# Performance work log

Measured on AMD Instinct MI355X. Metric: run time of the kernel, lower is better.

Reference implementation:

```python
import jax, jax.numpy as jnp
import numpy as np

HEADS = 4
DIM_HEAD = 32
SCALE = 10.0
EPS = 1e-12


def setup_inputs() -> dict:
    key = jax.random.key(0)
    k1, k2, k3 = jax.random.split(key, 3)
    B, D, H, W, C = 2, 8, 16, 32, 128
    dim = HEADS * DIM_HEAD  # 128
    x = jax.random.normal(k1, (B, D, H, W, C), dtype=jnp.float32)
    # 1x1x1 convs are matmuls over the channel dim
    w_qkv = jax.random.normal(k2, (C, 3 * dim), dtype=jnp.float32) * (1.0 / np.sqrt(C))
    w_out = jax.random.normal(k3, (dim, C), dtype=jnp.float32) * (1.0 / np.sqrt(dim))
    b_out = jnp.zeros((C,), dtype=jnp.float32)
    return {"x": x, "w_qkv": w_qkv, "w_out": w_out, "b_out": b_out}


def reference(x, w_qkv, w_out, b_out):
    B, D, H, W, C = x.shape
    N = D * H * W
    dim = HEADS * DIM_HEAD
    xf = x.reshape(B, N, C)
    qkv = xf @ w_qkv                                   # [B, N, 3*dim]
    q, k, v = jnp.split(qkv, 3, axis=-1)
    def to_heads(t):
        return t.reshape(B, N, HEADS, DIM_HEAD)        # [B, N, h, d]
    q, k, v = to_heads(q), to_heads(k), to_heads(v)
    # L2-normalize q and k along head dim (cosine attention)
    q = q / jnp.clip(jnp.linalg.norm(q, axis=-1, keepdims=True), EPS)
    k = k / jnp.clip(jnp.linalg.norm(k, axis=-1, keepdims=True), EPS)
    sim = jnp.einsum('bihd,bjhd->bhij', q, k) * SCALE  # [B, h, N, N]
    attn = jax.nn.softmax(sim, axis=-1)
    out = jnp.einsum('bhij,bjhd->bihd', attn, v)       # [B, N, h, d]
    out = out.reshape(B, N, dim)
    out = out @ w_out + b_out                          # [B, N, C]
    return out.reshape(B, D, H, W, C)
```

## Files before the change

### kernel.cpp

```cpp
#include <hip/hip_runtime.h>
#include <math.h>

#define HEADS   4
#define DH      32
#define NB      4096
#define BATCH   2
#define C_IN    128
#define QKV_COLS 384
#define TOTROWS 8192
#define ATT_EPS 1e-12f
#define C1      14.42695040888963f
#define QROWS   8
#define OROWS   8

typedef __attribute__((ext_vector_type(16))) float f32x16;
typedef _Float16 f16x8 __attribute__((ext_vector_type(8)));
typedef __fp16 fp16x2 __attribute__((ext_vector_type(2)));
typedef unsigned short u16;

__device__ __forceinline__ u16 f16b(float a) {
  union { _Float16 h; u16 u; } t; t.h = (_Float16)a; return t.u;
}
__device__ __forceinline__ unsigned pkf16rtn(float a, float b) {
  return (unsigned)f16b(a) | ((unsigned)f16b(b) << 16);
}
union Uh2 { fp16x2 h; unsigned u; };
__device__ __forceinline__ unsigned pkf16(float a, float b) {
  Uh2 t; t.h = __builtin_amdgcn_cvt_pkrtz(a, b); return t.u;
}
union U8h { unsigned u[4]; f16x8 h8; };
__device__ __forceinline__ f16x8 mk8h(unsigned a, unsigned b, unsigned c, unsigned d) {
  U8h t; t.u[0] = a; t.u[1] = b; t.u[2] = c; t.u[3] = d; return t.h8;
}
__device__ __forceinline__ void pl32swap(unsigned& a, unsigned& b) {
  asm("v_permlane32_swap_b32 %0, %1" : "+v"(a), "+v"(b));
}
#define GL16(gp, lp)                                                        \
  __builtin_amdgcn_global_load_lds(                                         \
      (const __attribute__((address_space(1))) void*)(gp),                  \
      (__attribute__((address_space(3))) void*)(lp), 16, 0, 0)

__global__ __launch_bounds__(384) void qkv_kernel(
    const float* __restrict__ x, const float* __restrict__ w,
    float* __restrict__ Qs, u16* __restrict__ K16, u16* __restrict__ VT16) {
  const int tid = threadIdx.x;
  const int r0  = blockIdx.x * QROWS;

  float4 a4[QROWS];
#pragma unroll
  for (int r = 0; r < QROWS; ++r) a4[r] = make_float4(0.f, 0.f, 0.f, 0.f);

  for (int c4 = 0; c4 < 32; ++c4) {
    const float wv0 = w[(c4 * 4 + 0) * QKV_COLS + tid];
    const float wv1 = w[(c4 * 4 + 1) * QKV_COLS + tid];
    const float wv2 = w[(c4 * 4 + 2) * QKV_COLS + tid];
    const float wv3 = w[(c4 * 4 + 3) * QKV_COLS + tid];
#pragma unroll
    for (int r = 0; r < QROWS; ++r) {
      const float* xr = x + (size_t)(r0 + r) * C_IN + c4 * 4;
      a4[r].x = fmaf(xr[0], wv0, a4[r].x);
      a4[r].y = fmaf(xr[1], wv1, a4[r].y);
      a4[r].z = fmaf(xr[2], wv2, a4[r].z);
      a4[r].w = fmaf(xr[3], wv3, a4[r].w);
    }
  }

  float acc[QROWS];
#pragma unroll
  for (int r = 0; r < QROWS; ++r)
    acc[r] = (a4[r].x + a4[r].y) + (a4[r].z + a4[r].w);

  const int part = tid >> 7;
  if (part < 2) {
#pragma unroll
    for (int r = 0; r < QROWS; ++r) {
      float s = acc[r] * acc[r];
      s += __shfl_xor(s, 1, 32);
      s += __shfl_xor(s, 2, 32);
      s += __shfl_xor(s, 4, 32);
      s += __shfl_xor(s, 8, 32);
      s += __shfl_xor(s, 16, 32);
      acc[r] *= 1.0f / fmaxf(sqrtf(s), ATT_EPS);
    }
  }

  const int h = (tid >> 5) & 3, d = tid & 31;
  const int b = r0 >> 12, n0 = r0 & (NB - 1);
  const int bh = b * HEADS + h;
  if (part == 0) {
    float* dst = Qs + ((size_t)bh * NB + n0) * DH + d;
#pragma unroll
    for (int r = 0; r < QROWS; ++r) dst[(size_t)r * DH] = acc[r] * C1;
  } else if (part == 1) {
    const size_t kb = ((size_t)bh * NB + n0) * DH + d;
#pragma unroll
    for (int r = 0; r < QROWS; ++r) K16[kb + (size_t)r * DH] = f16b(acc[r]);
  } else {
    const size_t vb = ((size_t)bh * DH + d) * NB + n0;
#pragma unroll
    for (int r = 0; r < QROWS; r += 4) {
      uint2 hv;
      hv.x = pkf16rtn(acc[r + 0], acc[r + 1]);
      hv.y = pkf16rtn(acc[r + 2], acc[r + 3]);
      *(uint2*)(VT16 + vb + r) = hv;
    }
  }
}

__global__ __launch_bounds__(512, 4) void attn_kernel(
    const float* __restrict__ Qs, const u16* __restrict__ K16,
    const u16* __restrict__ VT16, float* __restrict__ AO) {
  __shared__ __align__(16) char sbuf[2][4][2][2048];

  const int tid  = threadIdx.x;
  const int lane = tid & 63;
  const int w    = tid >> 6;
  const int su   = w & 3;
  const int u    = w >> 2;
  const int q    = lane & 31;
  const int hi   = lane >> 5;
  const int bh   = blockIdx.x & 7;
  const int qp   = blockIdx.x >> 3;

  const int nrow = qp * 64 + u * 32 + q;
  const float* qrow = Qs + ((size_t)bh * NB + nrow) * DH;
  f16x8 fq16[2];
#pragma unroll
  for (int sl = 0; sl < 2; ++sl) {
    const int d0 = sl * 16 + hi * 8;
    const float4 a = *(const float4*)(qrow + d0);
    const float4 b = *(const float4*)(qrow + d0 + 4);
    fq16[sl] = mk8h(pkf16rtn(a.x, a.y), pkf16rtn(a.z, a.w),
                    pkf16rtn(b.x, b.y), pkf16rtn(b.z, b.w));
  }

  const u16* gp[2]; int gst[2], ldso[2];
#pragma unroll
  for (int it = 0; it < 2; ++it) {
    const int i    = tid + it * 512;
    const int pidx = i >> 7;
    const int sp   = pidx >> 1;
    const int pl   = pidx & 1;
    const int s    = i & 127;
    const int rtt  = s >> 2;
    const int ps   = s & 3;
    const int slot = ((ps ^ ((rtt >> 1) & 3)) << 3);
    if (pl == 0) {
      gp[it]  = K16 + (size_t)bh * NB * DH + (size_t)(sp * 1024 + rtt) * DH + slot;
      gst[it] = 32 * DH;
    } else {
      gp[it]  = VT16 + (size_t)bh * DH * NB + (size_t)rtt * NB + sp * 1024 + slot;
      gst[it] = 32;
    }
    ldso[it] = i * 16;
  }
  char* const sb = (char*)sbuf;
  auto stage = [&](int buf) {
#pragma unroll
    for (int it = 0; it < 2; ++it) {
      GL16(gp[it], sb + buf * 16384 + ldso[it]);
      gp[it] += gst[it];
    }
  };

  const int swq = (q >> 1) & 3;
  int koff[2];
#pragma unroll
  for (int i = 0; i < 2; ++i) koff[i] = q * 64 + (((i * 2 + hi) ^ swq) << 4);

  f32x16 oa;
#pragma unroll
  for (int r = 0; r < 16; ++r) oa[r] = 0.f;
  float lrun = 0.f;

  stage(0);
  __syncthreads();

  for (int t = 0; t < 32; ++t) {
    const int cur = t & 1;
    if (t < 31) stage(cur ^ 1);

    const char* cb = sb + cur * 16384 + su * 4096;
    const char* ck = cb;
    const char* cv = cb + 2048;

    f32x16 sa;
#pragma unroll
    for (int r = 0; r < 16; ++r) sa[r] = 0.f;
    __builtin_amdgcn_s_setprio(1);
#pragma unroll
    for (int sl = 0; sl < 2; ++sl) {
      const f16x8 fk = *(const f16x8*)(ck + koff[sl]);
      sa = __builtin_amdgcn_mfma_f32_32x32x16_f16(fk, fq16[sl], sa, 0, 0, 0);
    }
    __builtin_amdgcn_s_setprio(0);

    float e[16], lsum = 0.f;
#pragma unroll
    for (int r = 0; r < 16; ++r) {
      e[r] = __builtin_amdgcn_exp2f(sa[r]);
      lsum += e[r];
    }
    lrun += lsum;

    __builtin_amdgcn_s_setprio(1);
#pragma unroll
    for (int m = 0; m < 2; ++m) {
      const float* eb = e + 8 * m;
      unsigned x0 = pkf16(eb[0], eb[1]), x1 = pkf16(eb[2], eb[3]);
      unsigned y0 = pkf16(eb[4], eb[5]), y1 = pkf16(eb[6], eb[7]);
      pl32swap(x0, y0);
      pl32swap(x1, y1);
      const f16x8 fP = mk8h(x0, x1, y0, y1);
      const f16x8 fv = *(const f16x8*)(cv + koff[m]);
      oa = __builtin_amdgcn_mfma_f32_32x32x16_f16(fv, fP, oa, 0, 0, 0);
    }
    __builtin_amdgcn_s_setprio(0);
    __syncthreads();
  }

  float* const mO = (float*)sbuf;
  float* const mL = mO + 2 * 3 * 32 * 33;
  const float Lfull = lrun + __shfl_xor(lrun, 32);
  if (su != 0) {
    const int sidx = (u * 3 + (su - 1)) * 32 + q;
    if (hi == 0) mL[sidx] = Lfull;
#pragma unroll
    for (int r = 0; r < 16; ++r) {
      const int d = (r & 3) + 8 * (r >> 2) + 4 * hi;
      mO[sidx * 33 + d] = oa[r];
    }
  }
  __syncthreads();
  if (su == 0) {
    float Lt = Lfull;
#pragma unroll
    for (int s = 0; s < 3; ++s) Lt += mL[(u * 3 + s) * 32 + q];
    const float inv = 1.0f / Lt;
    const int b = bh >> 2, h = bh & 3;
    float* dst = AO + ((size_t)(b * NB + nrow)) * 128 + h * DH;
#pragma unroll
    for (int r = 0; r < 16; ++r) {
      const int d = (r & 3) + 8 * (r >> 2) + 4 * hi;
      float v = oa[r];
#pragma unroll
      for (int s = 0; s < 3; ++s) v += mO[((u * 3 + s) * 32 + q) * 33 + d];
      dst[d] = v * inv;
    }
  }
}

__global__ __launch_bounds__(128) void outproj_kernel(
    const float* __restrict__ AO, const float* __restrict__ w,
    const float* __restrict__ bias, float* __restrict__ out) {
  const int tid = threadIdx.x;
  const int r0  = blockIdx.x * OROWS;

  float4 a4[OROWS];
#pragma unroll
  for (int r = 0; r < OROWS; ++r) a4[r] = make_float4(0.f, 0.f, 0.f, 0.f);

  for (int c4 = 0; c4 < 32; ++c4) {
    const float wv0 = w[(c4 * 4 + 0) * 128 + tid];
    const float wv1 = w[(c4 * 4 + 1) * 128 + tid];
    const float wv2 = w[(c4 * 4 + 2) * 128 + tid];
    const float wv3 = w[(c4 * 4 + 3) * 128 + tid];
#pragma unroll
    for (int r = 0; r < OROWS; ++r) {
      const float* xr = AO + (size_t)(r0 + r) * 128 + c4 * 4;
      a4[r].x = fmaf(xr[0], wv0, a4[r].x);
      a4[r].y = fmaf(xr[1], wv1, a4[r].y);
      a4[r].z = fmaf(xr[2], wv2, a4[r].z);
      a4[r].w = fmaf(xr[3], wv3, a4[r].w);
    }
  }

  __syncthreads();

  const float bv = bias[tid];
#pragma unroll
  for (int r = 0; r < OROWS; ++r) {
    const float acc = (a4[r].x + a4[r].y) + (a4[r].z + a4[r].w);
    out[(size_t)(r0 + r) * 128 + tid] = acc + bv;
  }
}

extern "C" void kernel_launch(void* const* d_in, const int* in_sizes, int n_in,
                              void* d_out, int out_size, void* d_ws, size_t ws_size,
                              hipStream_t stream) {
  (void)in_sizes; (void)n_in; (void)out_size; (void)ws_size;
  const float* x     = (const float*)d_in[0];
  const float* w_qkv = (const float*)d_in[1];
  const float* w_out = (const float*)d_in[2];
  const float* b_out = (const float*)d_in[3];
  float* out = (float*)d_out;

  float* ws = (float*)d_ws;
  float* Qs = ws;
  u16* K16  = (u16*)(ws + 1048576);
  u16* VT16 = K16 + 1048576;
  float* AO = out;

  qkv_kernel<<<TOTROWS / QROWS, 384, 0, stream>>>(x, w_qkv, Qs, K16, VT16);
  attn_kernel<<<512, 512, 0, stream>>>(Qs, K16, VT16, AO);
  outproj_kernel<<<TOTROWS / OROWS, 128, 0, stream>>>(AO, w_out, b_out, out);
}
```

Before: 67.83 us.

## Triple-buffer K/V staging with vmcnt waits and a single barrier per iteration

Moves the attention loop from a double-buffered LDS pipeline with two syncthreads per step to a three-slot ring. Two tiles are prefetched ahead, and each iteration waits with explicit s_waitcnt vmcnt plus one s_barrier. The goal is to hide global-to-LDS load latency better and cut barrier stalls. It also interleaves the P packing with the V MFMAs and starts the first QK MFMA from a zero register. The cost is 16 KB more LDS per block, which may reduce occupancy under launch_bounds(512,4), and the hand-counted vmcnt values assume a fixed number of loads per stage.

```diff
diff --git a/kernel.cpp b/kernel.cpp
--- a/kernel.cpp
+++ b/kernel.cpp
@@ -110,7 +110,7 @@
 __global__ __launch_bounds__(512, 4) void attn_kernel(
     const float* __restrict__ Qs, const u16* __restrict__ K16,
     const u16* __restrict__ VT16, float* __restrict__ AO) {
-  __shared__ __align__(16) char sbuf[2][4][2][2048];
+  __shared__ __align__(16) char sbuf[3][4][2][2048];
 
   const int tid  = threadIdx.x;
   const int lane = tid & 63;
@@ -168,30 +168,32 @@
 #pragma unroll
   for (int i = 0; i < 2; ++i) koff[i] = q * 64 + (((i * 2 + hi) ^ swq) << 4);
 
-  f32x16 oa;
-#pragma unroll
-  for (int r = 0; r < 16; ++r) oa[r] = 0.f;
+  f32x16 oa, zz;
+#pragma unroll
+  for (int r = 0; r < 16; ++r) { oa[r] = 0.f; zz[r] = 0.f; }
   float lrun = 0.f;
 
   stage(0);
-  __syncthreads();
+  stage(1);
 
   for (int t = 0; t < 32; ++t) {
-    const int cur = t & 1;
-    if (t < 31) stage(cur ^ 1);
-
-    const char* cb = sb + cur * 16384 + su * 4096;
+    if (t < 31) asm volatile("s_waitcnt vmcnt(2)" ::: "memory");
+    else        asm volatile("s_waitcnt vmcnt(0)" ::: "memory");
+    __builtin_amdgcn_sched_barrier(0);
+    __builtin_amdgcn_s_barrier();
+    __builtin_amdgcn_sched_barrier(0);
+
+    const char* cb = sb + (t % 3) * 16384 + su * 4096;
     const char* ck = cb;
     const char* cv = cb + 2048;
 
     f32x16 sa;
-#pragma unroll
-    for (int r = 0; r < 16; ++r) sa[r] = 0.f;
     __builtin_amdgcn_s_setprio(1);
-#pragma unroll
-    for (int sl = 0; sl < 2; ++sl) {
-      const f16x8 fk = *(const f16x8*)(ck + koff[sl]);
-      sa = __builtin_amdgcn_mfma_f32_32x32x16_f16(fk, fq16[sl], sa, 0, 0, 0);
+    {
+      const f16x8 fk0 = *(const f16x8*)(ck + koff[0]);
+      const f16x8 fk1 = *(const f16x8*)(ck + koff[1]);
+      sa = __builtin_amdgcn_mfma_f32_32x32x16_f16(fk0, fq16[0], zz, 0, 0, 0);
+      sa = __builtin_amdgcn_mfma_f32_32x32x16_f16(fk1, fq16[1], sa, 0, 0, 0);
     }
     __builtin_amdgcn_s_setprio(0);
 
@@ -204,21 +206,29 @@
     lrun += lsum;
 
     __builtin_amdgcn_s_setprio(1);
-#pragma unroll
-    for (int m = 0; m < 2; ++m) {
-      const float* eb = e + 8 * m;
-      unsigned x0 = pkf16(eb[0], eb[1]), x1 = pkf16(eb[2], eb[3]);
-      unsigned y0 = pkf16(eb[4], eb[5]), y1 = pkf16(eb[6], eb[7]);
+    {
+      unsigned x0 = pkf16(e[0], e[1]), x1 = pkf16(e[2], e[3]);
+      unsigned y0 = pkf16(e[4], e[5]), y1 = pkf16(e[6], e[7]);
       pl32swap(x0, y0);
       pl32swap(x1, y1);
-      const f16x8 fP = mk8h(x0, x1, y0, y1);
-      const f16x8 fv = *(const f16x8*)(cv + koff[m]);
-      oa = __builtin_amdgcn_mfma_f32_32x32x16_f16(fv, fP, oa, 0, 0, 0);
+      const f16x8 fv0 = *(const f16x8*)(cv + koff[0]);
+      oa = __builtin_amdgcn_mfma_f32_32x32x16_f16(fv0, mk8h(x0, x1, y0, y1),
+                                                  oa, 0, 0, 0);
+      unsigned z0 = pkf16(e[8], e[9]),   z1 = pkf16(e[10], e[11]);
+      unsigned t0 = pkf16(e[12], e[13]), t1 = pkf16(e[14], e[15]);
+      pl32swap(z0, t0);
+      pl32swap(z1, t1);
+      const f16x8 fv1 = *(const f16x8*)(cv + koff[1]);
+      oa = __builtin_amdgcn_mfma_f32_32x32x16_f16(fv1, mk8h(z0, z1, t0, t1),
+                                                  oa, 0, 0, 0);
     }
     __builtin_amdgcn_s_setprio(0);
-    __syncthreads();
-  }
-
+
+    if (t < 30) stage((t + 2) % 3);
+    __builtin_amdgcn_sched_barrier(0);
+  }
+
+  __syncthreads();
   float* const mO = (float*)sbuf;
   float* const mL = mO + 2 * 3 * 32 * 33;
   const float Lfull = lrun + __shfl_xor(lrun, 32);
```

Result: no change. 67.70 us (-0.2%).
